# Optimization experiments

Measured on AMD Instinct MI355X. Metric: run time of the kernel, lower is better.

Reference implementation:

```python
import jax, jax.numpy as jnp
import numpy as np

GROUP_SIZE = 128
HIDDEN = 2048
INTER = 5632
TOKENS = 8192
_SHIFTS = jnp.arange(8, dtype=jnp.uint32) * 4  # 4-bit nibbles, 8 per int32


def _pack_rows(nib):
    # nib: [in, out] int values in [0,16); pack 8 consecutive rows into one int32
    r, c = nib.shape
    n = nib.reshape(r // 8, 8, c).astype(jnp.uint32)
    packed = jnp.sum(n << _SHIFTS[None, :, None], axis=1, dtype=jnp.uint32)
    return jax.lax.bitcast_convert_type(packed, jnp.int32)  # [in//8, out]


def _pack_cols(nib):
    # nib: [groups, out]; pack 8 consecutive cols into one int32
    g, o = nib.shape
    n = nib.reshape(g, o // 8, 8).astype(jnp.uint32)
    packed = jnp.sum(n << _SHIFTS[None, None, :], axis=-1, dtype=jnp.uint32)
    return jax.lax.bitcast_convert_type(packed, jnp.int32)  # [groups, out//8]


def _dequant(qweight, qzeros, scales, group_size=GROUP_SIZE):
    # GPTQ int4 dequant: w = (q - (z + 1)) * scale, per group of `group_size` input rows
    in_packed, out = qweight.shape
    in_dim = in_packed * 8
    groups = scales.shape[0]
    sh = jnp.arange(8, dtype=jnp.int32) * 4
    q = (qweight[:, None, :] >> sh[None, :, None]) & 0xF       # [in//8, 8, out]
    q = q.reshape(in_dim, out)
    z = (qzeros[:, :, None] >> sh[None, None, :]) & 0xF        # [groups, out//8, 8]
    z = z.reshape(groups, out)
    gidx = jnp.arange(in_dim) // group_size                    # [in]
    w = (q - (z[gidx] + 1)).astype(scales.dtype) * scales[gidx]
    return w  # [in, out]


def setup_inputs() -> dict:
    key = jax.random.key(0)
    ks = jax.random.split(key, 10)
    x = jax.random.normal(ks[0], (TOKENS, HIDDEN), dtype=jnp.float32)

    def make(kq, kz, ksc, in_dim, out_dim):
        qn = jax.random.randint(kq, (in_dim, out_dim), 0, 16, dtype=jnp.int32)
        zn = jax.random.randint(kz, (in_dim // GROUP_SIZE, out_dim), 0, 16, dtype=jnp.int32)
        sc = jax.random.uniform(ksc, (in_dim // GROUP_SIZE, out_dim), jnp.float32, 1e-3, 2e-2)
        return _pack_rows(qn), _pack_cols(zn), sc

    gq, gz, gs = make(ks[1], ks[2], ks[3], HIDDEN, INTER)
    uq, uz, us = make(ks[4], ks[5], ks[6], HIDDEN, INTER)
    dq, dz, ds = make(ks[7], ks[8], ks[9], INTER, HIDDEN)
    return {
        "x": x,
        "gate_qweight": gq, "gate_qzeros": gz, "gate_scales": gs,
        "up_qweight": uq, "up_qzeros": uz, "up_scales": us,
        "down_qweight": dq, "down_qzeros": dz, "down_scales": ds,
    }


def reference(x, gate_qweight, gate_qzeros, gate_scales,
              up_qweight, up_qzeros, up_scales,
              down_qweight, down_qzeros, down_scales):
    wg = _dequant(gate_qweight, gate_qzeros, gate_scales)  # [H, I]
    wu = _dequant(up_qweight, up_qzeros, up_scales)        # [H, I]
    wd = _dequant(down_qweight, down_qzeros, down_scales)  # [I, H]
    # fused_gate_up: silu(x @ Wg) * (x @ Wu)
    h = jax.nn.silu(x @ wg) * (x @ wu)                     # [T, I]
    return h @ wd                                          # [T, H]
```

## Files before the change

kernel.cpp:

```cpp
#include <hip/hip_runtime.h>

#define TOKENS 8192
#define HIDDEN 2048
#define INTER  5632

typedef _Float16 f16x8 __attribute__((ext_vector_type(8)));
typedef float    f32x4 __attribute__((ext_vector_type(4)));

__device__ __forceinline__ void async_copy16(const void* g, void* l) {
  __builtin_amdgcn_global_load_lds(
      (const __attribute__((address_space(1))) unsigned int*)g,
      (__attribute__((address_space(3))) unsigned int*)l, 16, 0, 0);
}

__global__ void k_convert_x(const float* __restrict__ x, _Float16* __restrict__ xs) {
  const int kb = blockIdx.x;
  const int mt = blockIdx.y;
  const int m  = threadIdx.x;
  const float* src = x + (size_t)(mt * 128 + m) * HIDDEN + kb * 8;
  float4 f0 = *(const float4*)src;
  float4 f1 = *(const float4*)(src + 4);
  f16x8 v;
  v[0] = (_Float16)f0.x; v[1] = (_Float16)f0.y; v[2] = (_Float16)f0.z; v[3] = (_Float16)f0.w;
  v[4] = (_Float16)f1.x; v[5] = (_Float16)f1.y; v[6] = (_Float16)f1.z; v[7] = (_Float16)f1.w;
  *(f16x8*)(xs + ((size_t)(mt * 256 + kb) * 128 + m) * 8) = v;
}

__global__ void k_dequant(const unsigned int* __restrict__ qw,
                          const unsigned int* __restrict__ qz,
                          const float* __restrict__ sc,
                          _Float16* __restrict__ out, int N, int N8) {
  const int n  = blockIdx.x * 256 + threadIdx.x;
  const int k8 = blockIdx.y;
  const int g  = k8 >> 4;
  unsigned int q  = qw[(size_t)k8 * N + n];
  unsigned int zw = qz[(size_t)g * N8 + (n >> 3)];
  int   z1 = (int)((zw >> ((n & 7) * 4)) & 0xFu) + 1;
  float s  = sc[(size_t)g * N + n];
  f16x8 w;
#pragma unroll
  for (int j = 0; j < 8; ++j)
    w[j] = (_Float16)((float)((int)((q >> (4 * j)) & 0xFu) - z1) * s);
  *(f16x8*)(out + ((size_t)k8 * N + n) * 8) = w;
}

__global__ __launch_bounds__(256, 2)
void k_gemm_gateup(const _Float16* __restrict__ xs,
                   const _Float16* __restrict__ wg,
                   const _Float16* __restrict__ wu,
                   _Float16* __restrict__ hs) {
  __shared__ _Float16 lds[3 * 8192];
  _Float16* Al  = lds;
  _Float16* Bgl = lds + 8192;
  _Float16* Bul = lds + 16384;
  const int nt = blockIdx.x, mt = blockIdx.y;
  const int tid = threadIdx.x;
  const int wave = tid >> 6, lane = tid & 63;
  const int wm = wave >> 1, wn = wave & 1;
  const int row16 = lane >> 4, col = lane & 15;
  const int slot = wave * 4;

  const _Float16* gA = xs + (size_t)mt * 256 * 1024;

  int afo[4], bfo[4];
#pragma unroll
  for (int i = 0; i < 4; ++i) {
    afo[i] = (row16 * 128 + wm * 64 + i * 16 + col) * 8;
    bfo[i] = (row16 * 128 + wn * 64 + i * 16 + col) * 8;
  }

  const f32x4 zero = {0.f, 0.f, 0.f, 0.f};
  f32x4 accg[4][4], accu[4][4];
#pragma unroll
  for (int i = 0; i < 4; ++i)
#pragma unroll
    for (int j = 0; j < 4; ++j) { accg[i][j] = zero; accu[i][j] = zero; }

  for (int kit = 0; kit < HIDDEN / 64; ++kit) {
    __syncthreads();
#pragma unroll
    for (int q = 0; q < 4; ++q) {
      const int c = (slot + q) * 64 + lane;
      async_copy16(gA + (size_t)kit * 8192 + (size_t)c * 8,
                   (char*)Al + (size_t)(slot + q) * 1024);
      const int kbl = c >> 7, cc = c & 127;
      const size_t bo = ((size_t)(kit * 8 + kbl) * INTER + nt * 128 + cc) * 8;
      async_copy16(wg + bo, (char*)Bgl + (size_t)(slot + q) * 1024);
      async_copy16(wu + bo, (char*)Bul + (size_t)(slot + q) * 1024);
    }
    __syncthreads();
#pragma unroll
    for (int ks = 0; ks < 2; ++ks) {
      const int kadd = ks * 4096;
      f16x8 af[4], bg[4], bu[4];
#pragma unroll
      for (int i = 0; i < 4; ++i) {
        af[i] = *(const f16x8*)(Al  + kadd + afo[i]);
        bg[i] = *(const f16x8*)(Bgl + kadd + bfo[i]);
        bu[i] = *(const f16x8*)(Bul + kadd + bfo[i]);
      }
#pragma unroll
      for (int mi = 0; mi < 4; ++mi)
#pragma unroll
        for (int ni = 0; ni < 4; ++ni) {
          accg[mi][ni] = __builtin_amdgcn_mfma_f32_16x16x32_f16(af[mi], bg[ni], accg[mi][ni], 0, 0, 0);
          accu[mi][ni] = __builtin_amdgcn_mfma_f32_16x16x32_f16(af[mi], bu[ni], accu[mi][ni], 0, 0, 0);
        }
    }
  }
#pragma unroll
  for (int mi = 0; mi < 4; ++mi)
#pragma unroll
    for (int ni = 0; ni < 4; ++ni) {
      const int kg = nt * 128 + wn * 64 + ni * 16 + col;
      const size_t base = (size_t)(mt * (INTER / 8) + (kg >> 3)) * 1024 + (kg & 7);
#pragma unroll
      for (int r = 0; r < 4; ++r) {
        float g = accg[mi][ni][r], u = accu[mi][ni][r];
        float h = g / (1.f + __expf(-g)) * u;
        const int ml = wm * 64 + mi * 16 + row16 * 4 + r;
        hs[base + (size_t)ml * 8] = (_Float16)h;
      }
    }
}

__global__ __launch_bounds__(256, 2)
void k_gemm_down(const _Float16* __restrict__ hs,
                 const _Float16* __restrict__ wd,
                 float* __restrict__ out) {
  __shared__ _Float16 lds[2 * 8192];
  _Float16* Al = lds;
  _Float16* Bl = lds + 8192;
  const int nt = blockIdx.x, mt = blockIdx.y;
  const int tid = threadIdx.x;
  const int wave = tid >> 6, lane = tid & 63;
  const int wm = wave >> 1, wn = wave & 1;
  const int row16 = lane >> 4, col = lane & 15;
  const int slot = wave * 4;

  const _Float16* gA = hs + (size_t)mt * (INTER / 8) * 1024;

  int afo[4], bfo[4];
#pragma unroll
  for (int i = 0; i < 4; ++i) {
    afo[i] = (row16 * 128 + wm * 64 + i * 16 + col) * 8;
    bfo[i] = (row16 * 128 + wn * 64 + i * 16 + col) * 8;
  }

  const f32x4 zero = {0.f, 0.f, 0.f, 0.f};
  f32x4 acc[4][4];
#pragma unroll
  for (int i = 0; i < 4; ++i)
#pragma unroll
    for (int j = 0; j < 4; ++j) acc[i][j] = zero;

  for (int kit = 0; kit < INTER / 64; ++kit) {
    __syncthreads();
#pragma unroll
    for (int q = 0; q < 4; ++q) {
      const int c = (slot + q) * 64 + lane;
      async_copy16(gA + (size_t)kit * 8192 + (size_t)c * 8,
                   (char*)Al + (size_t)(slot + q) * 1024);
      const int kbl = c >> 7, cc = c & 127;
      const size_t bo = ((size_t)(kit * 8 + kbl) * HIDDEN + nt * 128 + cc) * 8;
      async_copy16(wd + bo, (char*)Bl + (size_t)(slot + q) * 1024);
    }
    __syncthreads();
#pragma unroll
    for (int ks = 0; ks < 2; ++ks) {
      const int kadd = ks * 4096;
      f16x8 af[4], bf[4];
#pragma unroll
      for (int i = 0; i < 4; ++i) {
        af[i] = *(const f16x8*)(Al + kadd + afo[i]);
        bf[i] = *(const f16x8*)(Bl + kadd + bfo[i]);
      }
#pragma unroll
      for (int mi = 0; mi < 4; ++mi)
#pragma unroll
        for (int ni = 0; ni < 4; ++ni)
          acc[mi][ni] = __builtin_amdgcn_mfma_f32_16x16x32_f16(af[mi], bf[ni], acc[mi][ni], 0, 0, 0);
    }
  }
#pragma unroll
  for (int mi = 0; mi < 4; ++mi)
#pragma unroll
    for (int ni = 0; ni < 4; ++ni) {
      const int n = nt * 128 + wn * 64 + ni * 16 + col;
#pragma unroll
      for (int r = 0; r < 4; ++r) {
        const int m = mt * 128 + wm * 64 + mi * 16 + row16 * 4 + r;
        out[(size_t)m * HIDDEN + n] = acc[mi][ni][r];
      }
    }
}

extern "C" void kernel_launch(void* const* d_in, const int* in_sizes, int n_in,
                              void* d_out, int out_size, void* d_ws, size_t ws_size,
                              hipStream_t stream) {
  (void)in_sizes; (void)n_in; (void)out_size; (void)ws_size;
  const float*        x  = (const float*)d_in[0];
  const unsigned int* gq = (const unsigned int*)d_in[1];
  const unsigned int* gz = (const unsigned int*)d_in[2];
  const float*        gs = (const float*)d_in[3];
  const unsigned int* uq = (const unsigned int*)d_in[4];
  const unsigned int* uz = (const unsigned int*)d_in[5];
  const float*        us = (const float*)d_in[6];
  const unsigned int* dq = (const unsigned int*)d_in[7];
  const unsigned int* dz = (const unsigned int*)d_in[8];
  const float*        ds = (const float*)d_in[9];
  float* out = (float*)d_out;

  char* ws = (char*)d_ws;
  _Float16* xs  = (_Float16*)ws;
  _Float16* wgd = (_Float16*)(ws + (size_t)TOKENS * HIDDEN * 2);
  _Float16* wud = wgd + (size_t)HIDDEN * INTER;
  _Float16* wdd = wud + (size_t)HIDDEN * INTER;
  _Float16* hs  = wdd + (size_t)INTER * HIDDEN;

  k_convert_x<<<dim3(HIDDEN / 8, TOKENS / 128), 128, 0, stream>>>(x, xs);
  k_dequant<<<dim3(INTER / 256, HIDDEN / 8), 256, 0, stream>>>(gq, gz, gs, wgd, INTER, INTER / 8);
  k_dequant<<<dim3(INTER / 256, HIDDEN / 8), 256, 0, stream>>>(uq, uz, us, wud, INTER, INTER / 8);
  k_dequant<<<dim3(HIDDEN / 256, INTER / 8), 256, 0, stream>>>(dq, dz, ds, wdd, HIDDEN, HIDDEN / 8);
  k_gemm_gateup<<<dim3(INTER / 128, TOKENS / 128), 256, 0, stream>>>(xs, wgd, wud, hs);
  k_gemm_down<<<dim3(HIDDEN / 128, TOKENS / 128), 256, 0, stream>>>(hs, wdd, out);
}
```

Measured before the change: 715.0 us.

## Fuse int4 dequantization into GEMM mainloops using magic-number fp16 conversion

```diff
diff --git a/kernel.cpp b/kernel.cpp
--- a/kernel.cpp
+++ b/kernel.cpp
@@ -1,16 +1,41 @@
 #include <hip/hip_runtime.h>
+#include <stdint.h>
 
 #define TOKENS 8192
 #define HIDDEN 2048
 #define INTER  5632
 
 typedef _Float16 f16x8 __attribute__((ext_vector_type(8)));
+typedef _Float16 f16x2 __attribute__((ext_vector_type(2)));
 typedef float    f32x4 __attribute__((ext_vector_type(4)));
+typedef unsigned int uint;
 
 __device__ __forceinline__ void async_copy16(const void* g, void* l) {
   __builtin_amdgcn_global_load_lds(
-      (const __attribute__((address_space(1))) unsigned int*)g,
-      (__attribute__((address_space(3))) unsigned int*)l, 16, 0, 0);
+      (const __attribute__((address_space(1))) uint*)g,
+      (__attribute__((address_space(3))) uint*)l, 16, 0, 0);
+}
+
+union U8 { uint u[4]; f16x8 v; };
+__device__ __forceinline__ f16x8 dq8(uint w, uint sd, uint zd) {
+  const f16x2 s = __builtin_bit_cast(f16x2, sd);
+  const f16x2 z = __builtin_bit_cast(f16x2, zd);
+  U8 r;
+  uint t0 = (w & 0x000F000Fu) | 0x64006400u;
+  uint t1 = ((w >> 4) & 0x000F000Fu) | 0x64006400u;
+  uint t2 = ((w >> 8) & 0x000F000Fu) | 0x64006400u;
+  uint t3 = ((w >> 12) & 0x000F000Fu) | 0x64006400u;
+  r.u[0] = __builtin_bit_cast(uint, (f16x2)((__builtin_bit_cast(f16x2, t0) - z) * s));
+  r.u[1] = __builtin_bit_cast(uint, (f16x2)((__builtin_bit_cast(f16x2, t1) - z) * s));
+  r.u[2] = __builtin_bit_cast(uint, (f16x2)((__builtin_bit_cast(f16x2, t2) - z) * s));
+  r.u[3] = __builtin_bit_cast(uint, (f16x2)((__builtin_bit_cast(f16x2, t3) - z) * s));
+  return r.v;
+}
+
+__device__ __forceinline__ uint dupf16(float x) {
+  _Float16 h = (_Float16)x;
+  unsigned short b = __builtin_bit_cast(unsigned short, h);
+  return (uint)b * 0x00010001u;
 }
 
 __global__ void k_convert_x(const float* __restrict__ x, _Float16* __restrict__ xs) {
@@ -21,38 +46,50 @@
   float4 f0 = *(const float4*)src;
   float4 f1 = *(const float4*)(src + 4);
   f16x8 v;
-  v[0] = (_Float16)f0.x; v[1] = (_Float16)f0.y; v[2] = (_Float16)f0.z; v[3] = (_Float16)f0.w;
-  v[4] = (_Float16)f1.x; v[5] = (_Float16)f1.y; v[6] = (_Float16)f1.z; v[7] = (_Float16)f1.w;
+  v[0] = (_Float16)f0.x; v[1] = (_Float16)f1.x;
+  v[2] = (_Float16)f0.y; v[3] = (_Float16)f1.y;
+  v[4] = (_Float16)f0.z; v[5] = (_Float16)f1.z;
+  v[6] = (_Float16)f0.w; v[7] = (_Float16)f1.w;
   *(f16x8*)(xs + ((size_t)(mt * 256 + kb) * 128 + m) * 8) = v;
 }
 
-__global__ void k_dequant(const unsigned int* __restrict__ qw,
-                          const unsigned int* __restrict__ qz,
-                          const float* __restrict__ sc,
-                          _Float16* __restrict__ out, int N, int N8) {
-  const int n  = blockIdx.x * 256 + threadIdx.x;
-  const int k8 = blockIdx.y;
-  const int g  = k8 >> 4;
-  unsigned int q  = qw[(size_t)k8 * N + n];
-  unsigned int zw = qz[(size_t)g * N8 + (n >> 3)];
-  int   z1 = (int)((zw >> ((n & 7) * 4)) & 0xFu) + 1;
-  float s  = sc[(size_t)g * N + n];
-  f16x8 w;
-#pragma unroll
-  for (int j = 0; j < 8; ++j)
-    w[j] = (_Float16)((float)((int)((q >> (4 * j)) & 0xFu) - z1) * s);
-  *(f16x8*)(out + ((size_t)k8 * N + n) * 8) = w;
+__global__ void k_prep_szgu(const uint* __restrict__ gz, const float* __restrict__ gs,
+                            const uint* __restrict__ uz, const float* __restrict__ us,
+                            uint4* __restrict__ out) {
+  const int n = blockIdx.x * 256 + threadIdx.x;
+  const int g = blockIdx.y;
+  const int sh = (n & 7) * 4;
+  int zg = (int)((gz[(size_t)g * (INTER / 8) + (n >> 3)] >> sh) & 0xFu);
+  int zu = (int)((uz[(size_t)g * (INTER / 8) + (n >> 3)] >> sh) & 0xFu);
+  float sg = gs[(size_t)g * INTER + n];
+  float su = us[(size_t)g * INTER + n];
+  out[(size_t)g * INTER + n] =
+      make_uint4(dupf16(sg), dupf16((float)(1025 + zg)),
+                 dupf16(su), dupf16((float)(1025 + zu)));
+}
+
+__global__ void k_prep_szd(const uint* __restrict__ dz, const float* __restrict__ ds,
+                           uint2* __restrict__ out) {
+  const int n = blockIdx.x * 256 + threadIdx.x;
+  const int g = blockIdx.y;
+  const int sh = (n & 7) * 4;
+  int z = (int)((dz[(size_t)g * (HIDDEN / 8) + (n >> 3)] >> sh) & 0xFu);
+  float s = ds[(size_t)g * HIDDEN + n];
+  out[(size_t)g * HIDDEN + n] = make_uint2(dupf16(s), dupf16((float)(1025 + z)));
 }
 
 __global__ __launch_bounds__(256, 2)
 void k_gemm_gateup(const _Float16* __restrict__ xs,
-                   const _Float16* __restrict__ wg,
-                   const _Float16* __restrict__ wu,
+                   const uint* __restrict__ gq,
+                   const uint* __restrict__ uq,
+                   const uint4* __restrict__ szgu,
                    _Float16* __restrict__ hs) {
-  __shared__ _Float16 lds[3 * 8192];
-  _Float16* Al  = lds;
-  _Float16* Bgl = lds + 8192;
-  _Float16* Bul = lds + 16384;
+  __shared__ char smem[16384 + 4096 + 4096 + 2048];
+  _Float16* Al = (_Float16*)smem;
+  char* Bgl = smem + 16384;
+  char* Bul = smem + 20480;
+  char* szl = smem + 24576;
+
   const int nt = blockIdx.x, mt = blockIdx.y;
   const int tid = threadIdx.x;
   const int wave = tid >> 6, lane = tid & 63;
@@ -62,12 +99,19 @@
 
   const _Float16* gA = xs + (size_t)mt * 256 * 1024;
 
-  int afo[4], bfo[4];
-#pragma unroll
-  for (int i = 0; i < 4; ++i) {
+  const int brow = 2 * wave + (lane >> 5);
+  const int bcolw = ((lane & 31) * 4) ^ ((brow & 1) << 4);
+  const size_t bbase = (size_t)brow * INTER + nt * 128 + bcolw;
+
+  int afo[4];
+#pragma unroll
+  for (int i = 0; i < 4; ++i)
     afo[i] = (row16 * 128 + wm * 64 + i * 16 + col) * 8;
-    bfo[i] = (row16 * 128 + wn * 64 + i * 16 + col) * 8;
-  }
+  int bco[4];
+  const int bswz = (row16 & 1) << 4;
+#pragma unroll
+  for (int ni = 0; ni < 4; ++ni)
+    bco[ni] = (wn * 64 + ni * 16 + col) ^ bswz;
 
   const f32x4 zero = {0.f, 0.f, 0.f, 0.f};
   f32x4 accg[4][4], accu[4][4];
@@ -76,35 +120,61 @@
 #pragma unroll
     for (int j = 0; j < 4; ++j) { accg[i][j] = zero; accu[i][j] = zero; }
 
+  uint2 szg[4], szu[4];
+
   for (int kit = 0; kit < HIDDEN / 64; ++kit) {
     __syncthreads();
 #pragma unroll
     for (int q = 0; q < 4; ++q) {
-      const int c = (slot + q) * 64 + lane;
-      async_copy16(gA + (size_t)kit * 8192 + (size_t)c * 8,
-                   (char*)Al + (size_t)(slot + q) * 1024);
-      const int kbl = c >> 7, cc = c & 127;
-      const size_t bo = ((size_t)(kit * 8 + kbl) * INTER + nt * 128 + cc) * 8;
-      async_copy16(wg + bo, (char*)Bgl + (size_t)(slot + q) * 1024);
-      async_copy16(wu + bo, (char*)Bul + (size_t)(slot + q) * 1024);
+      const int c2 = (slot + q) * 64 + lane;
+      async_copy16(gA + (size_t)kit * 8192 + (size_t)c2 * 8,
+                   (char*)Al + (slot + q) * 1024);
+    }
+    {
+      const size_t go = (size_t)kit * 8 * INTER + bbase;
+      async_copy16(gq + go, Bgl + wave * 1024);
+      async_copy16(uq + go, Bul + wave * 1024);
+    }
+    if (((kit & 1) == 0) && wave < 2) {
+      const int n = wave * 64 + lane;
+      async_copy16(szgu + (size_t)(kit >> 1) * INTER + nt * 128 + n,
+                   szl + wave * 1024);
     }
     __syncthreads();
+    if ((kit & 1) == 0) {
+#pragma unroll
+      for (int ni = 0; ni < 4; ++ni) {
+        const int n16 = (wn * 64 + ni * 16 + col) * 16;
+        szg[ni] = *(const uint2*)(szl + n16);
+        szu[ni] = *(const uint2*)(szl + n16 + 8);
+      }
+    }
 #pragma unroll
     for (int ks = 0; ks < 2; ++ks) {
       const int kadd = ks * 4096;
-      f16x8 af[4], bg[4], bu[4];
-#pragma unroll
-      for (int i = 0; i < 4; ++i) {
-        af[i] = *(const f16x8*)(Al  + kadd + afo[i]);
-        bg[i] = *(const f16x8*)(Bgl + kadd + bfo[i]);
-        bu[i] = *(const f16x8*)(Bul + kadd + bfo[i]);
+      f16x8 af[4];
+#pragma unroll
+      for (int i = 0; i < 4; ++i)
+        af[i] = *(const f16x8*)(Al + kadd + afo[i]);
+      const int bks = (ks * 4 + row16) * 512;
+      uint bgw[4], buw[4];
+#pragma unroll
+      for (int ni = 0; ni < 4; ++ni) {
+        bgw[ni] = *(const uint*)(Bgl + bks + bco[ni] * 4);
+        buw[ni] = *(const uint*)(Bul + bks + bco[ni] * 4);
+      }
+      f16x8 bgf[4], buf_[4];
+#pragma unroll
+      for (int ni = 0; ni < 4; ++ni) {
+        bgf[ni] = dq8(bgw[ni], szg[ni].x, szg[ni].y);
+        buf_[ni] = dq8(buw[ni], szu[ni].x, szu[ni].y);
       }
 #pragma unroll
       for (int mi = 0; mi < 4; ++mi)
 #pragma unroll
         for (int ni = 0; ni < 4; ++ni) {
-          accg[mi][ni] = __builtin_amdgcn_mfma_f32_16x16x32_f16(af[mi], bg[ni], accg[mi][ni], 0, 0, 0);
-          accu[mi][ni] = __builtin_amdgcn_mfma_f32_16x16x32_f16(af[mi], bu[ni], accu[mi][ni], 0, 0, 0);
+          accg[mi][ni] = __builtin_amdgcn_mfma_f32_16x16x32_f16(af[mi], bgf[ni], accg[mi][ni], 0, 0, 0);
+          accu[mi][ni] = __builtin_amdgcn_mfma_f32_16x16x32_f16(af[mi], buf_[ni], accu[mi][ni], 0, 0, 0);
         }
     }
   }
@@ -113,7 +183,9 @@
 #pragma unroll
     for (int ni = 0; ni < 4; ++ni) {
       const int kg = nt * 128 + wn * 64 + ni * 16 + col;
-      const size_t base = (size_t)(mt * (INTER / 8) + (kg >> 3)) * 1024 + (kg & 7);
+      const int sub = kg & 7;
+      const int pslot = ((sub & 3) << 1) | (sub >> 2);
+      const size_t base = (size_t)(mt * (INTER / 8) + (kg >> 3)) * 1024 + pslot;
 #pragma unroll
       for (int r = 0; r < 4; ++r) {
         float g = accg[mi][ni][r], u = accu[mi][ni][r];
@@ -126,11 +198,14 @@
 
 __global__ __launch_bounds__(256, 2)
 void k_gemm_down(const _Float16* __restrict__ hs,
-                 const _Float16* __restrict__ wd,
+                 const uint* __restrict__ dq,
+                 const uint2* __restrict__ szd,
                  float* __restrict__ out) {
-  __shared__ _Float16 lds[2 * 8192];
-  _Float16* Al = lds;
-  _Float16* Bl = lds + 8192;
+  __shared__ char smem[16384 + 4096 + 1024];
+  _Float16* Al = (_Float16*)smem;
+  char* Bl  = smem + 16384;
+  char* szl = smem + 20480;
+
   const int nt = blockIdx.x, mt = blockIdx.y;
   const int tid = threadIdx.x;
   const int wave = tid >> 6, lane = tid & 63;
@@ -140,12 +215,19 @@
 
   const _Float16* gA = hs + (size_t)mt * (INTER / 8) * 1024;
 
-  int afo[4], bfo[4];
-#pragma unroll
-  for (int i = 0; i < 4; ++i) {
+  const int brow = 2 * wave + (lane >> 5);
+  const int bcolw = ((lane & 31) * 4) ^ ((brow & 1) << 4);
+  const size_t bbase = (size_t)brow * HIDDEN + nt * 128 + bcolw;
+
+  int afo[4];
+#pragma unroll
+  for (int i = 0; i < 4; ++i)
     afo[i] = (row16 * 128 + wm * 64 + i * 16 + col) * 8;
-    bfo[i] = (row16 * 128 + wn * 64 + i * 16 + col) * 8;
-  }
+  int bco[4];
+  const int bswz = (row16 & 1) << 4;
+#pragma unroll
+  for (int ni = 0; ni < 4; ++ni)
+    bco[ni] = (wn * 64 + ni * 16 + col) ^ bswz;
 
   const f32x4 zero = {0.f, 0.f, 0.f, 0.f};
   f32x4 acc[4][4];
@@ -154,27 +236,44 @@
 #pragma unroll
     for (int j = 0; j < 4; ++j) acc[i][j] = zero;
 
+  uint2 sz[4];
+
   for (int kit = 0; kit < INTER / 64; ++kit) {
     __syncthreads();
 #pragma unroll
     for (int q = 0; q < 4; ++q) {
-      const int c = (slot + q) * 64 + lane;
-      async_copy16(gA + (size_t)kit * 8192 + (size_t)c * 8,
-                   (char*)Al + (size_t)(slot + q) * 1024);
-      const int kbl = c >> 7, cc = c & 127;
-      const size_t bo = ((size_t)(kit * 8 + kbl) * HIDDEN + nt * 128 + cc) * 8;
-      async_copy16(wd + bo, (char*)Bl + (size_t)(slot + q) * 1024);
+      const int c2 = (slot + q) * 64 + lane;
+      async_copy16(gA + (size_t)kit * 8192 + (size_t)c2 * 8,
+                   (char*)Al + (slot + q) * 1024);
+    }
+    async_copy16(dq + (size_t)kit * 8 * HIDDEN + bbase, Bl + wave * 1024);
+    if (((kit & 1) == 0) && wave == 0) {
+      async_copy16(szd + (size_t)(kit >> 1) * HIDDEN + nt * 128 + lane * 2, szl);
     }
     __syncthreads();
+    if ((kit & 1) == 0) {
+#pragma unroll
+      for (int ni = 0; ni < 4; ++ni) {
+        const int n8 = (wn * 64 + ni * 16 + col) * 8;
+        sz[ni] = *(const uint2*)(szl + n8);
+      }
+    }
 #pragma unroll
     for (int ks = 0; ks < 2; ++ks) {
       const int kadd = ks * 4096;
-      f16x8 af[4], bf[4];
-#pragma unroll
-      for (int i = 0; i < 4; ++i) {
+      f16x8 af[4];
+#pragma unroll
+      for (int i = 0; i < 4; ++i)
         af[i] = *(const f16x8*)(Al + kadd + afo[i]);
-        bf[i] = *(const f16x8*)(Bl + kadd + bfo[i]);
-      }
+      const int bks = (ks * 4 + row16) * 512;
+      uint bw[4];
+#pragma unroll
+      for (int ni = 0; ni < 4; ++ni)
+        bw[ni] = *(const uint*)(Bl + bks + bco[ni] * 4);
+      f16x8 bf[4];
+#pragma unroll
+      for (int ni = 0; ni < 4; ++ni)
+        bf[ni] = dq8(bw[ni], sz[ni].x, sz[ni].y);
 #pragma unroll
       for (int mi = 0; mi < 4; ++mi)
 #pragma unroll
@@ -199,29 +298,27 @@
                               void* d_out, int out_size, void* d_ws, size_t ws_size,
                               hipStream_t stream) {
   (void)in_sizes; (void)n_in; (void)out_size; (void)ws_size;
-  const float*        x  = (const float*)d_in[0];
-  const unsigned int* gq = (const unsigned int*)d_in[1];
-  const unsigned int* gz = (const unsigned int*)d_in[2];
-  const float*        gs = (const float*)d_in[3];
-  const unsigned int* uq = (const unsigned int*)d_in[4];
-  const unsigned int* uz = (const unsigned int*)d_in[5];
-  const float*        us = (const float*)d_in[6];
-  const unsigned int* dq = (const unsigned int*)d_in[7];
-  const unsigned int* dz = (const unsigned int*)d_in[8];
-  const float*        ds = (const float*)d_in[9];
+  const float* x  = (const float*)d_in[0];
+  const uint*  gq = (const uint*)d_in[1];
+  const uint*  gz = (const uint*)d_in[2];
+  const float* gs = (const float*)d_in[3];
+  const uint*  uq = (const uint*)d_in[4];
+  const uint*  uz = (const uint*)d_in[5];
+  const float* us = (const float*)d_in[6];
+  const uint*  dq = (const uint*)d_in[7];
+  const uint*  dz = (const uint*)d_in[8];
+  const float* ds = (const float*)d_in[9];
   float* out = (float*)d_out;
 
   char* ws = (char*)d_ws;
   _Float16* xs  = (_Float16*)ws;
-  _Float16* wgd = (_Float16*)(ws + (size_t)TOKENS * HIDDEN * 2);
-  _Float16* wud = wgd + (size_t)HIDDEN * INTER;
-  _Float16* wdd = wud + (size_t)HIDDEN * INTER;
-  _Float16* hs  = wdd + (size_t)INTER * HIDDEN;
+  _Float16* hs  = (_Float16*)(ws + (size_t)TOKENS * HIDDEN * 2);
+  uint4* szgu = (uint4*)(ws + (size_t)TOKENS * HIDDEN * 2 + (size_t)TOKENS * INTER * 2);
+  uint2* szd  = (uint2*)((char*)szgu + (size_t)16 * INTER * 16);
 
   k_convert_x<<<dim3(HIDDEN / 8, TOKENS / 128), 128, 0, stream>>>(x, xs);
-  k_dequant<<<dim3(INTER / 256, HIDDEN / 8), 256, 0, stream>>>(gq, gz, gs, wgd, INTER, INTER / 8);
-  k_dequant<<<dim3(INTER / 256, HIDDEN / 8), 256, 0, stream>>>(uq, uz, us, wud, INTER, INTER / 8);
-  k_dequant<<<dim3(HIDDEN / 256, INTER / 8), 256, 0, stream>>>(dq, dz, ds, wdd, HIDDEN, HIDDEN / 8);
-  k_gemm_gateup<<<dim3(INTER / 128, TOKENS / 128), 256, 0, stream>>>(xs, wgd, wud, hs);
-  k_gemm_down<<<dim3(HIDDEN / 128, TOKENS / 128), 256, 0, stream>>>(hs, wdd, out);
-}
+  k_prep_szgu<<<dim3(INTER / 256, HIDDEN / 128), 256, 0, stream>>>(gz, gs, uz, us, szgu);
+  k_prep_szd<<<dim3(HIDDEN / 256, INTER / 128), 256, 0, stream>>>(dz, ds, szd);
+  k_gemm_gateup<<<dim3(INTER / 128, TOKENS / 128), 256, 0, stream>>>(xs, gq, uq, szgu, hs);
+  k_gemm_down<<<dim3(HIDDEN / 128, TOKENS / 128), 256, 0, stream>>>(hs, dq, szd, out);
+}
```

After: 776.7 us. 1.09x slower.
